# Performance work log

Hardware: AMD Instinct MI355X
Metric: run time of the kernel (lower is better)

Reference implementation:

```python
import jax, jax.numpy as jnp
import numpy as np

D_MODEL = 1024
N_HEAD = 16


def setup_inputs() -> dict:
    key = jax.random.key(0)
    ks = jax.random.split(key, 12)
    B, T, D = 2, 2048, D_MODEL
    s = 1.0 / np.sqrt(D)
    return {
        "q": jax.random.normal(ks[0], (B, T, D), jnp.float32),
        "k": jax.random.normal(ks[1], (B, T, D), jnp.float32),
        "v": jax.random.normal(ks[2], (B, T, D), jnp.float32),
        "w_q": jax.random.normal(ks[3], (D, D), jnp.float32) * s,
        "b_q": jnp.zeros((D,), jnp.float32),
        "w_k": jax.random.normal(ks[4], (D, D), jnp.float32) * s,
        "b_k": jnp.zeros((D,), jnp.float32),
        "w_v": jax.random.normal(ks[5], (D, D), jnp.float32) * s,
        "b_v": jnp.zeros((D,), jnp.float32),
        "w_o": jax.random.normal(ks[6], (D, D), jnp.float32) * s,
        "b_o": jnp.zeros((D,), jnp.float32),
    }


def reference(q, k, v, w_q, b_q, w_k, b_k, w_v, b_v, w_o, b_o):
    B, T, D = q.shape
    H = N_HEAD
    nd = D // H  # head dim
    # projections (weights stored as [in, out])
    qh = (q @ w_q + b_q).reshape(B, T, H, nd).transpose(0, 2, 1, 3)  # [b,h,t,nd]
    kh = (k @ w_k + b_k).reshape(B, T, H, nd).transpose(0, 2, 1, 3)
    vh = (v @ w_v + b_v).reshape(B, T, H, nd).transpose(0, 2, 1, 3)
    score = jnp.einsum('bhqd,bhkd->bhqk', qh, kh) / jnp.sqrt(jnp.float32(nd))
    causal = jnp.tril(jnp.ones((T, T), dtype=bool))  # [tq, tk]
    score = jnp.where(causal, score, -jnp.inf)
    # NOTE: original module uses nn.Softmax(dim=-2), i.e. softmax over the
    # QUERY axis. Faithful to the source.
    attn = jax.nn.softmax(score, axis=-2)
    out = jnp.einsum('bhqk,bhkd->bhqd', attn, vh)  # [b,h,t,nd]
    out = out.transpose(0, 2, 1, 3).reshape(B, T, D)
    return out @ w_o + b_o
```

## Files before the change

kernel.cpp:

```cpp
#include <hip/hip_runtime.h>
#include <hip/hip_bf16.h>
#include <cstdint>
#include <cstddef>

#define D_MODEL 1024
#define NHEAD   16
#define HDIM    64
#define BB      2
#define TT      2048
#define MM      (BB*TT)
#define BHN     (BB*NHEAD)

typedef __attribute__((ext_vector_type(8))) __bf16 bf16x8;
typedef __attribute__((ext_vector_type(4))) float  f32x4;
typedef __attribute__((ext_vector_type(8))) unsigned short u16x8;
typedef __attribute__((ext_vector_type(4))) unsigned short u16x4;

__device__ __forceinline__ unsigned short f2b(float f){
  __bf16 b = (__bf16)f;
  return __builtin_bit_cast(unsigned short, b);
}
__device__ __forceinline__ float b2f(unsigned short u){
  unsigned int x = ((unsigned int)u) << 16;
  return __builtin_bit_cast(float, x);
}

__device__ __forceinline__ f32x4 mfma16(bf16x8 a, bf16x8 b, f32x4 c){
  return __builtin_amdgcn_mfma_f32_16x16x32_bf16(a, b, c, 0, 0, 0);
}

__device__ __forceinline__ void gload16(const void* g, void* lds){
  __builtin_amdgcn_global_load_lds((const __attribute__((address_space(1))) void*)g,
                                   (__attribute__((address_space(3))) void*)lds, 16, 0, 0);
}

__global__ void transpose_w_kernel(const float* __restrict__ W0, const float* __restrict__ W1,
                                   const float* __restrict__ W2, const float* __restrict__ W3,
                                   unsigned short* __restrict__ T0, unsigned short* __restrict__ T1,
                                   unsigned short* __restrict__ T2, unsigned short* __restrict__ T3){
  __shared__ float tile[32][33];
  const int z = blockIdx.z;
  const float* W = z==0 ? W0 : z==1 ? W1 : z==2 ? W2 : W3;
  unsigned short* Wt = z==0 ? T0 : z==1 ? T1 : z==2 ? T2 : T3;
  int tx = threadIdx.x, ty = threadIdx.y;
  int x0 = blockIdx.x*32, y0 = blockIdx.y*32;
  #pragma unroll
  for (int i=0;i<4;i++)
    tile[ty + i*8][tx] = W[(size_t)(y0 + ty + i*8)*D_MODEL + x0 + tx];
  __syncthreads();
  #pragma unroll
  for (int i=0;i<4;i++)
    Wt[(size_t)(x0 + ty + i*8)*D_MODEL + y0 + tx] = f2b(tile[tx][ty + i*8]);
}

__device__ __forceinline__ void gemm_body_f32A(const float* __restrict__ A,
                                               const unsigned short* __restrict__ Bt,
                                               const float* __restrict__ bias,
                                               void* __restrict__ Cout, const int mode,
                                               const int m0, const int n0)
{
  constexpr int K = D_MODEL, N = D_MODEL;
  __shared__ unsigned short As[2][128*32];
  __shared__ unsigned short Bs[2][128*32];
  const int t = threadIdx.x, lane = t&63, w = t>>6;
  const int wr = w>>1, wc = w&1, lr = lane&15, lg = lane>>4;
  const int srow = lane>>2;
  const int schunk = (lane&3) ^ ((lane>>3)&3);
  const int ra = t>>1, half = t&1;
  const int u0 = (half*2)     ^ ((ra>>1)&3);
  const int u1 = (half*2 + 1) ^ ((ra>>1)&3);
  const int crd = lg ^ ((lr>>1)&3);
  f32x4 acc[4][4] = {};
  float4 a0,a1,a2,a3;

  auto loadA = [&](int k0){
    const float4* pa = (const float4*)(A + (size_t)(m0+ra)*K + k0 + half*16);
    a0=pa[0]; a1=pa[1]; a2=pa[2]; a3=pa[3];
  };
  auto writeA = [&](int buf){
    u16x8 p0, p1;
    p0[0]=f2b(a0.x); p0[1]=f2b(a0.y); p0[2]=f2b(a0.z); p0[3]=f2b(a0.w);
    p0[4]=f2b(a1.x); p0[5]=f2b(a1.y); p0[6]=f2b(a1.z); p0[7]=f2b(a1.w);
    p1[0]=f2b(a2.x); p1[1]=f2b(a2.y); p1[2]=f2b(a2.z); p1[3]=f2b(a2.w);
    p1[4]=f2b(a3.x); p1[5]=f2b(a3.y); p1[6]=f2b(a3.z); p1[7]=f2b(a3.w);
    *(u16x8*)((char*)As[buf] + ra*64 + u0*16) = p0;
    *(u16x8*)((char*)As[buf] + ra*64 + u1*16) = p1;
  };
  auto stageB = [&](int buf, int k0){
    #pragma unroll
    for (int g=0; g<2; g++){
      int reg = w*2 + g;
      int r = reg*16 + srow;
      gload16(Bt + (size_t)(n0+r)*K + k0 + schunk*8, (char*)Bs[buf] + reg*1024);
    }
  };

  loadA(0); stageB(0, 0); writeA(0);
  __syncthreads();
  int buf = 0;
  for (int ks = 0; ks < 32; ++ks){
    if (ks < 31){ loadA((ks+1)*32); stageB(buf^1, (ks+1)*32); }
    const char* bufA = (const char*)As[buf];
    const char* bufB = (const char*)Bs[buf];
    bf16x8 af[4], bfv[4];
    #pragma unroll
    for (int mi=0;mi<4;mi++){
      int r = wr*64 + mi*16 + lr;
      af[mi] = *(const bf16x8*)(bufA + r*64 + crd*16);
    }
    #pragma unroll
    for (int ni=0;ni<4;ni++){
      int r = wc*64 + ni*16 + lr;
      bfv[ni] = *(const bf16x8*)(bufB + r*64 + crd*16);
    }
    #pragma unroll
    for (int mi=0;mi<4;mi++)
      #pragma unroll
      for (int ni=0;ni<4;ni++)
        acc[mi][ni] = mfma16(af[mi], bfv[ni], acc[mi][ni]);
    if (ks < 31) writeA(buf^1);
    __syncthreads();
    buf ^= 1;
  }

  #pragma unroll
  for (int mi=0;mi<4;mi++){
    #pragma unroll
    for (int ni=0;ni<4;ni++){
      int n = n0 + wc*64 + ni*16 + lr;
      int mbase = m0 + wr*64 + mi*16 + lg*4;
      float bv = bias[n];
      if (mode == 0){
        unsigned short* Cb = (unsigned short*)Cout;
        #pragma unroll
        for (int r=0;r<4;r++) Cb[(size_t)(mbase+r)*N + n] = f2b(acc[mi][ni][r] + bv);
      } else {
        unsigned short* Vt = (unsigned short*)Cout;
        int h = n >> 6, d = n & 63;
        int b = mbase >> 11;
        int tq = mbase & (TT-1);
        u16x4 vv;
        #pragma unroll
        for (int r=0;r<4;r++) vv[r] = f2b(acc[mi][ni][r] + bv);
        *(u16x4*)(Vt + ((size_t)((b*NHEAD + h)*HDIM + d))*TT + tq) = vv;
      }
    }
  }
}

__launch_bounds__(256)
__global__ void proj_gemm_kernel(const float* __restrict__ q,
                                 const float* __restrict__ k,
                                 const float* __restrict__ v,
                                 const unsigned short* __restrict__ Wtq,
                                 const unsigned short* __restrict__ Wtk,
                                 const unsigned short* __restrict__ Wtv,
                                 const float* __restrict__ b_q, const float* __restrict__ b_k,
                                 const float* __restrict__ b_v,
                                 unsigned short* __restrict__ Qb, unsigned short* __restrict__ Kb,
                                 unsigned short* __restrict__ Vt)
{
  const int id = blockIdx.x;
  const int xcd = id & 7, r2 = id >> 3;
  const int n = r2 & 7, mz = r2 >> 3;
  const int m = (mz & 3)*8 + xcd, z = mz >> 2;
  const float* A  = z==0 ? q : z==1 ? k : v;
  const unsigned short* Bt = z==0 ? Wtq : z==1 ? Wtk : Wtv;
  const float* bias = z==0 ? b_q : z==1 ? b_k : b_v;
  void* C = z==0 ? (void*)Qb : z==1 ? (void*)Kb : (void*)Vt;
  gemm_body_f32A(A, Bt, bias, C, z==2 ? 1 : 0, m*128, n*128);
}

__launch_bounds__(256)
__global__ void out_gemm_kernel(const unsigned short* __restrict__ Ob,
                                const unsigned short* __restrict__ Wto,
                                const float* __restrict__ b_o, float* __restrict__ out)
{
  constexpr int K = D_MODEL, N = D_MODEL;
  __shared__ unsigned short As[2][64*32];
  __shared__ unsigned short Bs[2][128*32];
  const int id = blockIdx.x;
  const int xcd = id & 7, r2 = id >> 3;
  const int n0 = (r2 & 7)*128, m0 = ((r2 >> 3)*8 + xcd)*64;
  const int t = threadIdx.x, lane = t&63, w = t>>6;
  const int wr = w>>1, wc = w&1, lr = lane&15, lg = lane>>4;
  const int srow = lane>>2;
  const int schunk = (lane&3) ^ ((lane>>3)&3);
  const int crd = lg ^ ((lr>>1)&3);
  f32x4 acc[2][4] = {};

  auto stage = [&](int buf, int k0){
    { int r = w*16 + srow;
      gload16(Ob + (size_t)(m0+r)*K + k0 + schunk*8, (char*)As[buf] + w*1024); }
    #pragma unroll
    for (int g=0; g<2; g++){
      int reg = w*2 + g;
      int r = reg*16 + srow;
      gload16(Wto + (size_t)(n0+r)*K + k0 + schunk*8, (char*)Bs[buf] + reg*1024);
    }
  };

  stage(0, 0);
  __syncthreads();
  int buf = 0;
  for (int ks = 0; ks < 32; ++ks){
    if (ks < 31) stage(buf^1, (ks+1)*32);
    const char* bufA = (const char*)As[buf];
    const char* bufB = (const char*)Bs[buf];
    bf16x8 af[2], bfv[4];
    #pragma unroll
    for (int mi=0;mi<2;mi++){
      int r = wr*32 + mi*16 + lr;
      af[mi] = *(const bf16x8*)(bufA + r*64 + crd*16);
    }
    #pragma unroll
    for (int ni=0;ni<4;ni++){
      int r = wc*64 + ni*16 + lr;
      bfv[ni] = *(const bf16x8*)(bufB + r*64 + crd*16);
    }
    #pragma unroll
    for (int mi=0;mi<2;mi++)
      #pragma unroll
      for (int ni=0;ni<4;ni++)
        acc[mi][ni] = mfma16(af[mi], bfv[ni], acc[mi][ni]);
    __syncthreads();
    buf ^= 1;
  }

  #pragma unroll
  for (int mi=0;mi<2;mi++){
    #pragma unroll
    for (int ni=0;ni<4;ni++){
      int n = n0 + wc*64 + ni*16 + lr;
      int mbase = m0 + wr*32 + mi*16 + lg*4;
      float bv = b_o[n];
      #pragma unroll
      for (int r=0;r<4;r++) out[(size_t)(mbase+r)*N + n] = acc[mi][ni][r] + bv;
    }
  }
}

__launch_bounds__(256)
__global__ void col_stats_kernel(const unsigned short* __restrict__ Qb,
                                 const unsigned short* __restrict__ Kb,
                                 float* __restrict__ partialS)
{
  __shared__ unsigned short Ks[128*64];
  __shared__ unsigned short Qs[2][64*64];
  const int t = threadIdx.x, lane = t&63, w = t>>6;
  const int id = blockIdx.x;
  const int bh = id & 31, pair = id >> 5;
  const int kb_ = pair & 15, qc = pair >> 4;
  const int b = bh >> 4, h = bh & 15;
  const int k0 = kb_ * 128;
  const int lr = lane&15, lg = lane>>4;
  const int osrc = (lane&7) ^ (lane>>3);

  auto stageQ = [&](int buf, int qt){
    #pragma unroll
    for (int g=0; g<2; g++){
      int reg = w*2 + g;
      int r = reg*8 + (lane>>3);
      gload16(Qb + ((size_t)(b*TT + qt + r))*D_MODEL + h*64 + osrc*8,
              (char*)Qs[buf] + reg*1024);
    }
  };

  const int qstart = (k0 > qc*256) ? k0 : qc*256;
  const int qend   = (qc+1)*256;

  #pragma unroll
  for (int g=0; g<4; g++){
    int reg = w*4 + g;
    int r = reg*8 + (lane>>3);
    gload16(Kb + ((size_t)(b*TT + k0 + r))*D_MODEL + h*64 + osrc*8, (char*)Ks + reg*1024);
  }
  if (qstart < qend) stageQ(0, qstart);
  __syncthreads();

  bf16x8 bk[2][2];
  #pragma unroll
  for (int kb=0;kb<2;kb++)
    #pragma unroll
    for (int ks=0;ks<2;ks++){
      int r = w*32 + kb*16 + lr;
      bk[kb][ks] = *(const bf16x8*)((const char*)Ks + r*128 + (((ks*4+lg) ^ (r&7))*16));
    }
  f32x4 sacc[2] = {};
  int buf = 0;
  for (int qt = qstart; qt < qend; qt += 64){
    if (qt + 64 < qend) stageQ(buf^1, qt+64);
    const char* bufQ = (const char*)Qs[buf];
    const bool interior = (qt >= k0 + 128);
    #pragma unroll
    for (int qb=0;qb<4;qb++){
      bf16x8 aq[2];
      #pragma unroll
      for (int ks=0;ks<2;ks++){
        int r = qb*16 + lr;
        aq[ks] = *(const bf16x8*)(bufQ + r*128 + (((ks*4+lg) ^ (r&7))*16));
      }
      f32x4 sf[2] = {};
      #pragma unroll
      for (int ks=0;ks<2;ks++)
        #pragma unroll
        for (int kb=0;kb<2;kb++)
          sf[kb] = mfma16(aq[ks], bk[kb][ks], sf[kb]);
      #pragma unroll
      for (int kb=0;kb<2;kb++){
        int col = k0 + w*32 + kb*16 + lr;
        #pragma unroll
        for (int r=0;r<4;r++){
          float e = __expf(sf[kb][r] * 0.125f);
          if (!interior){
            int qg = qt + qb*16 + lg*4 + r;
            e = (qg >= col) ? e : 0.f;
          }
          sacc[kb][r] += e;
        }
      }
    }
    __syncthreads();
    buf ^= 1;
  }
  #pragma unroll
  for (int kb=0;kb<2;kb++){
    float s = sacc[kb][0] + sacc[kb][1] + sacc[kb][2] + sacc[kb][3];
    s += __shfl_xor(s, 16);
    s += __shfl_xor(s, 32);
    if (lg == 0){
      int col = k0 + w*32 + kb*16 + lr;
      partialS[((size_t)qc*BHN + bh)*TT + col] = s;
    }
  }
}

__global__ void col_combine_vscale_kernel(const float* __restrict__ partialS,
                                          unsigned short* __restrict__ Vt){
  const int bh = blockIdx.x >> 3, tc = blockIdx.x & 7;
  const int col = tc*256 + threadIdx.x;
  float s = 0.f;
  #pragma unroll
  for (int qc=0;qc<8;qc++) s += partialS[((size_t)qc*BHN + bh)*TT + col];
  const float inv = 1.0f / s;
  #pragma unroll 8
  for (int d=0; d<HDIM; d++){
    size_t idx = ((size_t)(bh*HDIM + d))*TT + col;
    Vt[idx] = f2b(b2f(Vt[idx]) * inv);
  }
}

__launch_bounds__(512)
__global__ void attn_out_kernel(const unsigned short* __restrict__ Qb,
                                const unsigned short* __restrict__ Kb,
                                const unsigned short* __restrict__ Vt,
                                unsigned short* __restrict__ O)
{
  __shared__ unsigned short Qs[128*64];
  __shared__ unsigned short Ks2[2][64*64];
  __shared__ unsigned short Vs[2][64*64];
  __shared__ unsigned short Ps[128*64];
  const int t = threadIdx.x, lane=t&63, w=t>>6;
  const int id = blockIdx.x;
  const int bh = id & 31;
  const int qi = 15 - (id >> 5);
  const int b = bh>>4, h = bh&15;
  const int q0 = qi*128;
  const int lr = lane&15, lg = lane>>4;
  const int osrc = (lane&7) ^ (lane>>3);

  auto stageKV = [&](int buf, int k0){
    int r = w*8 + (lane>>3);
    gload16(Kb + ((size_t)(b*TT + k0 + r))*D_MODEL + h*64 + osrc*8,
            (char*)Ks2[buf] + w*1024);
    gload16(Vt + ((size_t)(bh*HDIM + r))*TT + k0 + osrc*8,
            (char*)Vs[buf] + w*1024);
  };

  #pragma unroll
  for (int g=0; g<2; g++){
    int reg = w*2 + g;
    int r = reg*8 + (lane>>3);
    gload16(Qb + ((size_t)(b*TT + q0 + r))*D_MODEL + h*64 + osrc*8, (char*)Qs + reg*1024);
  }
  stageKV(0, 0);
  __syncthreads();

  bf16x8 aq[2];
  #pragma unroll
  for (int ks=0;ks<2;ks++){
    int r = w*16 + lr;
    aq[ks] = *(const bf16x8*)((const char*)Qs + r*128 + (((ks*4+lg) ^ (r&7))*16));
  }
  f32x4 oacc[4] = {};
  const int nkt = 2*qi + 2;
  int buf = 0;
  for (int kt=0; kt<nkt; kt++){
    int k0 = kt*64;
    if (kt+1 < nkt) stageKV(buf^1, k0+64);
    const bool active = (k0 <= q0 + w*16 + 15);
    if (active){
      const char* bufK = (const char*)Ks2[buf];
      const char* bufV = (const char*)Vs[buf];
      f32x4 sf[4] = {};
      __builtin_amdgcn_s_setprio(1);
      #pragma unroll
      for (int ks=0;ks<2;ks++)
        #pragma unroll
        for (int kb=0;kb<4;kb++){
          int r = kb*16 + lr;
          bf16x8 bk = *(const bf16x8*)(bufK + r*128 + (((ks*4+lg) ^ (r&7))*16));
          sf[kb] = mfma16(bk, aq[ks], sf[kb]);
        }
      __builtin_amdgcn_s_setprio(0);
      const bool boundary = (k0 + 64 > q0 + w*16);
      const int prow = w*16 + lr;
      #pragma unroll
      for (int kb=0;kb<4;kb++){
        u16x4 vv;
        #pragma unroll
        for (int r=0;r<4;r++){
          float pv = __expf(sf[kb][r]*0.125f);
          if (boundary){
            int kg = k0 + kb*16 + lg*4 + r;
            int qg = q0 + prow;
            pv = (qg >= kg) ? pv : 0.f;
          }
          vv[r] = f2b(pv);
        }
        *(u16x4*)((char*)Ps + ((prow*128 + kb*32 + lg*8) ^ ((prow&7)<<4))) = vv;
      }
      __builtin_amdgcn_s_setprio(1);
      #pragma unroll
      for (int ks=0;ks<2;ks++){
        bf16x8 pa = *(const bf16x8*)((const char*)Ps + prow*128 + (((ks*4+lg) ^ (prow&7))*16));
        #pragma unroll
        for (int db=0;db<4;db++){
          int r = db*16 + lr;
          bf16x8 bv = *(const bf16x8*)(bufV + r*128 + (((ks*4+lg) ^ (r&7))*16));
          oacc[db] = mfma16(pa, bv, oacc[db]);
        }
      }
      __builtin_amdgcn_s_setprio(0);
    }
    __syncthreads();
    buf ^= 1;
  }
  #pragma unroll
  for (int db=0;db<4;db++){
    int qg = q0 + w*16 + lg*4;
    int d  = db*16 + lr;
    #pragma unroll
    for (int r=0;r<4;r++)
      O[((size_t)(b*TT + qg + r))*D_MODEL + h*64 + d] = f2b(oacc[db][r]);
  }
}

extern "C" void kernel_launch(void* const* d_in, const int* in_sizes, int n_in,
                              void* d_out, int out_size, void* d_ws, size_t ws_size,
                              hipStream_t stream)
{
  (void)in_sizes; (void)n_in; (void)out_size; (void)ws_size;
  const float* q   = (const float*)d_in[0];
  const float* k   = (const float*)d_in[1];
  const float* v   = (const float*)d_in[2];
  const float* w_q = (const float*)d_in[3];
  const float* b_q = (const float*)d_in[4];
  const float* w_k = (const float*)d_in[5];
  const float* b_k = (const float*)d_in[6];
  const float* w_v = (const float*)d_in[7];
  const float* b_v = (const float*)d_in[8];
  const float* w_o = (const float*)d_in[9];
  const float* b_o = (const float*)d_in[10];

  char* p = (char*)d_ws;
  auto carve = [&](size_t bytes)->char* {
    char* r = p; p += (bytes + 255) & ~(size_t)255; return r;
  };
  unsigned short* Wtq = (unsigned short*)carve((size_t)D_MODEL*D_MODEL*2);
  unsigned short* Wtk = (unsigned short*)carve((size_t)D_MODEL*D_MODEL*2);
  unsigned short* Wtv = (unsigned short*)carve((size_t)D_MODEL*D_MODEL*2);
  unsigned short* Wto = (unsigned short*)carve((size_t)D_MODEL*D_MODEL*2);
  unsigned short* Qb  = (unsigned short*)carve((size_t)MM*D_MODEL*2);
  unsigned short* Kb  = (unsigned short*)carve((size_t)MM*D_MODEL*2);
  unsigned short* Vt  = (unsigned short*)carve((size_t)MM*D_MODEL*2);
  unsigned short* Ob  = (unsigned short*)carve((size_t)MM*D_MODEL*2);
  float* partialS = (float*)carve((size_t)8*BHN*TT*4);

  dim3 tgrid(32,32,4), tblk(32,8);
  transpose_w_kernel<<<tgrid, tblk, 0, stream>>>(w_q, w_k, w_v, w_o, Wtq, Wtk, Wtv, Wto);

  proj_gemm_kernel<<<dim3(768), 256, 0, stream>>>(q, k, v, Wtq, Wtk, Wtv,
                                                  b_q, b_k, b_v, Qb, Kb, Vt);

  col_stats_kernel<<<dim3(8*16*BHN), 256, 0, stream>>>(Qb, Kb, partialS);
  col_combine_vscale_kernel<<<dim3(BHN*8), 256, 0, stream>>>(partialS, Vt);

  attn_out_kernel<<<dim3((TT/128)*BHN), 512, 0, stream>>>(Qb, Kb, Vt, Ob);

  out_gemm_kernel<<<dim3(512), 256, 0, stream>>>(Ob, Wto, b_o, (float*)d_out);
}
```

Baseline: 151.7 us.

## Pre-convert activations to bf16 and triple-buffer projection GEMM with direct LDS loads

Adds a separate kernel that converts the q/k/v fp32 activations to bf16 in workspace. The projection GEMM then stages both A and B tiles with global-to-LDS direct loads into a three-deep buffer ring. It uses explicit vmcnt waits and raw barriers in place of __syncthreads, so loads run two stages ahead. This removes per-tile register conversion and halves A-operand bytes in the GEMM, at the cost of an extra pass that reads 48MB and writes 24MB, plus more LDS per block.

```diff
diff --git a/kernel.cpp b/kernel.cpp
--- a/kernel.cpp
+++ b/kernel.cpp
@@ -32,6 +32,22 @@
 __device__ __forceinline__ void gload16(const void* g, void* lds){
   __builtin_amdgcn_global_load_lds((const __attribute__((address_space(1))) void*)g,
                                    (__attribute__((address_space(3))) void*)lds, 16, 0, 0);
+}
+
+__global__ void cvt_bf16_kernel(const float* __restrict__ q, const float* __restrict__ k,
+                                const float* __restrict__ v,
+                                unsigned short* __restrict__ Xq, unsigned short* __restrict__ Xk,
+                                unsigned short* __restrict__ Xv){
+  const int z = blockIdx.y;
+  const float* x = z==0 ? q : z==1 ? k : v;
+  unsigned short* y = z==0 ? Xq : z==1 ? Xk : Xv;
+  size_t i = (size_t)blockIdx.x*blockDim.x + threadIdx.x;
+  const float4* p = (const float4*)(x + i*8);
+  float4 a = p[0], b = p[1];
+  u16x8 o;
+  o[0]=f2b(a.x); o[1]=f2b(a.y); o[2]=f2b(a.z); o[3]=f2b(a.w);
+  o[4]=f2b(b.x); o[5]=f2b(b.y); o[6]=f2b(b.z); o[7]=f2b(b.w);
+  *(u16x8*)(y + i*8) = o;
 }
 
 __global__ void transpose_w_kernel(const float* __restrict__ W0, const float* __restrict__ W1,
@@ -53,55 +69,46 @@
     Wt[(size_t)(x0 + ty + i*8)*D_MODEL + y0 + tx] = f2b(tile[tx][ty + i*8]);
 }
 
-__device__ __forceinline__ void gemm_body_f32A(const float* __restrict__ A,
-                                               const unsigned short* __restrict__ Bt,
-                                               const float* __restrict__ bias,
-                                               void* __restrict__ Cout, const int mode,
-                                               const int m0, const int n0)
+__device__ __forceinline__ void gemm_body(const unsigned short* __restrict__ A,
+                                          const unsigned short* __restrict__ Bt,
+                                          const float* __restrict__ bias,
+                                          void* __restrict__ Cout, const int mode,
+                                          const int m0, const int n0)
 {
   constexpr int K = D_MODEL, N = D_MODEL;
-  __shared__ unsigned short As[2][128*32];
-  __shared__ unsigned short Bs[2][128*32];
+  __shared__ unsigned short As[3][128*32];
+  __shared__ unsigned short Bs[3][128*32];
   const int t = threadIdx.x, lane = t&63, w = t>>6;
   const int wr = w>>1, wc = w&1, lr = lane&15, lg = lane>>4;
   const int srow = lane>>2;
   const int schunk = (lane&3) ^ ((lane>>3)&3);
-  const int ra = t>>1, half = t&1;
-  const int u0 = (half*2)     ^ ((ra>>1)&3);
-  const int u1 = (half*2 + 1) ^ ((ra>>1)&3);
   const int crd = lg ^ ((lr>>1)&3);
   f32x4 acc[4][4] = {};
-  float4 a0,a1,a2,a3;
-
-  auto loadA = [&](int k0){
-    const float4* pa = (const float4*)(A + (size_t)(m0+ra)*K + k0 + half*16);
-    a0=pa[0]; a1=pa[1]; a2=pa[2]; a3=pa[3];
-  };
-  auto writeA = [&](int buf){
-    u16x8 p0, p1;
-    p0[0]=f2b(a0.x); p0[1]=f2b(a0.y); p0[2]=f2b(a0.z); p0[3]=f2b(a0.w);
-    p0[4]=f2b(a1.x); p0[5]=f2b(a1.y); p0[6]=f2b(a1.z); p0[7]=f2b(a1.w);
-    p1[0]=f2b(a2.x); p1[1]=f2b(a2.y); p1[2]=f2b(a2.z); p1[3]=f2b(a2.w);
-    p1[4]=f2b(a3.x); p1[5]=f2b(a3.y); p1[6]=f2b(a3.z); p1[7]=f2b(a3.w);
-    *(u16x8*)((char*)As[buf] + ra*64 + u0*16) = p0;
-    *(u16x8*)((char*)As[buf] + ra*64 + u1*16) = p1;
-  };
-  auto stageB = [&](int buf, int k0){
+
+  auto stage = [&](int buf, int ks){
+    int k0 = ks*32;
     #pragma unroll
     for (int g=0; g<2; g++){
       int reg = w*2 + g;
       int r = reg*16 + srow;
+      gload16(A  + (size_t)(m0+r)*K + k0 + schunk*8, (char*)As[buf] + reg*1024);
       gload16(Bt + (size_t)(n0+r)*K + k0 + schunk*8, (char*)Bs[buf] + reg*1024);
     }
   };
 
-  loadA(0); stageB(0, 0); writeA(0);
-  __syncthreads();
-  int buf = 0;
+  stage(0, 0);
+  stage(1, 1);
+  asm volatile("s_waitcnt vmcnt(4)" ::: "memory");
+  asm volatile("s_barrier" ::: "memory");
+
+  int bi = 0;
   for (int ks = 0; ks < 32; ++ks){
-    if (ks < 31){ loadA((ks+1)*32); stageB(buf^1, (ks+1)*32); }
-    const char* bufA = (const char*)As[buf];
-    const char* bufB = (const char*)Bs[buf];
+    if (ks + 2 < 32){
+      int nb = bi + 2; if (nb >= 3) nb -= 3;
+      stage(nb, ks+2);
+    }
+    const char* bufA = (const char*)As[bi];
+    const char* bufB = (const char*)Bs[bi];
     bf16x8 af[4], bfv[4];
     #pragma unroll
     for (int mi=0;mi<4;mi++){
@@ -118,9 +125,10 @@
       #pragma unroll
       for (int ni=0;ni<4;ni++)
         acc[mi][ni] = mfma16(af[mi], bfv[ni], acc[mi][ni]);
-    if (ks < 31) writeA(buf^1);
-    __syncthreads();
-    buf ^= 1;
+    if (ks < 30) asm volatile("s_waitcnt vmcnt(4)" ::: "memory");
+    else         asm volatile("s_waitcnt vmcnt(0)" ::: "memory");
+    asm volatile("s_barrier" ::: "memory");
+    bi = (bi == 2) ? 0 : bi + 1;
   }
 
   #pragma unroll
@@ -149,9 +157,9 @@
 }
 
 __launch_bounds__(256)
-__global__ void proj_gemm_kernel(const float* __restrict__ q,
-                                 const float* __restrict__ k,
-                                 const float* __restrict__ v,
+__global__ void proj_gemm_kernel(const unsigned short* __restrict__ Xq,
+                                 const unsigned short* __restrict__ Xk,
+                                 const unsigned short* __restrict__ Xv,
                                  const unsigned short* __restrict__ Wtq,
                                  const unsigned short* __restrict__ Wtk,
                                  const unsigned short* __restrict__ Wtv,
@@ -164,11 +172,11 @@
   const int xcd = id & 7, r2 = id >> 3;
   const int n = r2 & 7, mz = r2 >> 3;
   const int m = (mz & 3)*8 + xcd, z = mz >> 2;
-  const float* A  = z==0 ? q : z==1 ? k : v;
+  const unsigned short* A  = z==0 ? Xq : z==1 ? Xk : Xv;
   const unsigned short* Bt = z==0 ? Wtq : z==1 ? Wtk : Wtv;
   const float* bias = z==0 ? b_q : z==1 ? b_k : b_v;
   void* C = z==0 ? (void*)Qb : z==1 ? (void*)Kb : (void*)Vt;
-  gemm_body_f32A(A, Bt, bias, C, z==2 ? 1 : 0, m*128, n*128);
+  gemm_body(A, Bt, bias, C, z==2 ? 1 : 0, m*128, n*128);
 }
 
 __launch_bounds__(256)
@@ -477,6 +485,9 @@
   auto carve = [&](size_t bytes)->char* {
     char* r = p; p += (bytes + 255) & ~(size_t)255; return r;
   };
+  unsigned short* Xq  = (unsigned short*)carve((size_t)MM*D_MODEL*2);
+  unsigned short* Xk  = (unsigned short*)carve((size_t)MM*D_MODEL*2);
+  unsigned short* Xv  = (unsigned short*)carve((size_t)MM*D_MODEL*2);
   unsigned short* Wtq = (unsigned short*)carve((size_t)D_MODEL*D_MODEL*2);
   unsigned short* Wtk = (unsigned short*)carve((size_t)D_MODEL*D_MODEL*2);
   unsigned short* Wtv = (unsigned short*)carve((size_t)D_MODEL*D_MODEL*2);
@@ -487,10 +498,12 @@
   unsigned short* Ob  = (unsigned short*)carve((size_t)MM*D_MODEL*2);
   float* partialS = (float*)carve((size_t)8*BHN*TT*4);
 
+  cvt_bf16_kernel<<<dim3((MM*D_MODEL/8)/256, 3), 256, 0, stream>>>(q, k, v, Xq, Xk, Xv);
+
   dim3 tgrid(32,32,4), tblk(32,8);
   transpose_w_kernel<<<tgrid, tblk, 0, stream>>>(w_q, w_k, w_v, w_o, Wtq, Wtk, Wtv, Wto);
 
-  proj_gemm_kernel<<<dim3(768), 256, 0, stream>>>(q, k, v, Wtq, Wtk, Wtv,
+  proj_gemm_kernel<<<dim3(768), 256, 0, stream>>>(Xq, Xk, Xv, Wtq, Wtk, Wtv,
                                                   b_q, b_k, b_v, Qb, Kb, Vt);
 
   col_stats_kernel<<<dim3(8*16*BHN), 256, 0, stream>>>(Qb, Kb, partialS);
```

New measurement: 147.3 us. 2.9% less time.
